# Kernel tuning notes

Hardware: AMD Instinct MI355X
Metric: run time of the kernel (lower is better)

Reference implementation:

```python
import jax, jax.numpy as jnp
import numpy as np

E = 800000
N = 50000
D = 128


def setup_inputs() -> dict:
    key = jax.random.key(0)
    k1, k2, k3, k4, k5 = jax.random.split(key, 5)
    messages = jax.random.normal(k1, (E, D), dtype=jnp.float32)
    dst_index = jax.random.randint(k2, (E,), 0, N, dtype=jnp.int32)
    h_prev = jax.random.normal(k3, (N, D), dtype=jnp.float32)
    # nn.Linear(5*D, D): weight [D, 5*D], bias [D]
    bound = 1.0 / np.sqrt(5 * D)
    W = jax.random.uniform(k4, (D, 5 * D), minval=-bound, maxval=bound, dtype=jnp.float32)
    b = jax.random.uniform(k5, (D,), minval=-bound, maxval=bound, dtype=jnp.float32)
    return {"messages": messages, "dst_index": dst_index, "h_prev": h_prev, "W": W, "b": b}


def reference(messages, dst_index, h_prev, W, b):
    n = h_prev.shape[0]
    ones = jnp.ones((messages.shape[0],), dtype=messages.dtype)
    count = jax.ops.segment_sum(ones, dst_index, num_segments=n)[:, None]       # [N,1]
    count_clamped = jnp.maximum(count, 1.0)
    sum_msg = jax.ops.segment_sum(messages, dst_index, num_segments=n)          # [N,D]
    mean_msg = sum_msg / count_clamped
    has_edge = count > 0
    # torch_scatter fills empty segments with 0 for max/min; segment_max/min give +/-inf
    max_msg = jnp.where(has_edge, jax.ops.segment_max(messages, dst_index, num_segments=n), 0.0)
    min_msg = jnp.where(has_edge, jax.ops.segment_min(messages, dst_index, num_segments=n), 0.0)
    sum_sq = jax.ops.segment_sum(messages * messages, dst_index, num_segments=n)
    mean_sq = sum_sq / count_clamped
    var = jnp.maximum(mean_sq - mean_msg * mean_msg, 1e-6)
    std_msg = jnp.sqrt(var)
    agg_feat = jnp.concatenate([mean_msg, max_msg, min_msg, std_msg, h_prev], axis=-1)  # [N,5D]
    return agg_feat @ W.T + b
```

## Files before the change

kernel.cpp:

```cpp
#include <hip/hip_runtime.h>
#include <hip/hip_bf16.h>
#include <cstdint>
#include <cstddef>

typedef unsigned short u16;
typedef __attribute__((ext_vector_type(8))) short short8;
typedef __attribute__((ext_vector_type(4))) float f32x4;

#define D_FEAT 128
#define CAP 64
#define NPB 32
#define ASTR 520

__global__ void zero_ints_kernel(int* __restrict__ a, int n) {
    int i = blockIdx.x * blockDim.x + threadIdx.x;
    int stride = gridDim.x * blockDim.x;
    for (; i < n; i += stride) a[i] = 0;
}

__global__ void wcvt_kernel(const float* __restrict__ W, u16* __restrict__ Wb, int n4) {
    int i = blockIdx.x * blockDim.x + threadIdx.x;
    if (i >= n4) return;
    float4 v = reinterpret_cast<const float4*>(W)[i];
    u16 o[4];
    float vv[4] = {v.x, v.y, v.z, v.w};
    #pragma unroll
    for (int t = 0; t < 4; ++t) {
        __hip_bfloat16 h = __float2bfloat16(vv[t]);
        o[t] = *reinterpret_cast<u16*>(&h);
    }
    reinterpret_cast<ushort2*>(Wb)[2 * i]     = make_ushort2(o[0], o[1]);
    reinterpret_cast<ushort2*>(Wb)[2 * i + 1] = make_ushort2(o[2], o[3]);
}

__global__ void scatter_kernel(const int* __restrict__ dst, int* __restrict__ cursor,
                               int* __restrict__ slots, int E) {
    int i = blockIdx.x * blockDim.x + threadIdx.x;
    int stride = gridDim.x * blockDim.x;
    for (; i < E; i += stride) {
        int d = dst[i];
        int p = atomicAdd(&cursor[d], 1);
        if (p < CAP) slots[(size_t)d * CAP + p] = i;
    }
}

__global__ __launch_bounds__(256) void fused_agg_gemm(
    const float* __restrict__ messages,
    const float* __restrict__ h_prev,
    const int* __restrict__ slots,
    const int* __restrict__ cursor,
    const u16* __restrict__ Wb,
    const float* __restrict__ bias,
    float* __restrict__ out,
    int N) {
    __shared__ __align__(16) u16 st[NPB * ASTR];

    const int wave = threadIdx.x >> 6;
    const int lane = threadIdx.x & 63;
    const int nb = blockIdx.x * NPB;

    for (int t = 0; t < NPB / 4; ++t) {
        const int nd = nb + wave * (NPB / 4) + t;
        if (nd >= N) break;
        const int cntT = cursor[nd];
        const int m = cntT < CAP ? cntT : CAP;
        const int* sl = slots + (size_t)nd * CAP;
        int eid = (lane < m) ? sl[lane] : 0;

        float s0 = 0.f, s1 = 0.f, q0 = 0.f, q1 = 0.f;
        float mx0 = -INFINITY, mx1 = -INFINITY, mn0 = INFINITY, mn1 = INFINITY;

        int i = 0;
        for (; i + 4 <= m; i += 4) {
            int e0 = __shfl(eid, i + 0, 64);
            int e1 = __shfl(eid, i + 1, 64);
            int e2 = __shfl(eid, i + 2, 64);
            int e3 = __shfl(eid, i + 3, 64);
            float2 v0 = *reinterpret_cast<const float2*>(messages + (size_t)e0 * D_FEAT + 2 * lane);
            float2 v1 = *reinterpret_cast<const float2*>(messages + (size_t)e1 * D_FEAT + 2 * lane);
            float2 v2 = *reinterpret_cast<const float2*>(messages + (size_t)e2 * D_FEAT + 2 * lane);
            float2 v3 = *reinterpret_cast<const float2*>(messages + (size_t)e3 * D_FEAT + 2 * lane);
            s0 += v0.x; q0 = fmaf(v0.x, v0.x, q0); mx0 = fmaxf(mx0, v0.x); mn0 = fminf(mn0, v0.x);
            s1 += v0.y; q1 = fmaf(v0.y, v0.y, q1); mx1 = fmaxf(mx1, v0.y); mn1 = fminf(mn1, v0.y);
            s0 += v1.x; q0 = fmaf(v1.x, v1.x, q0); mx0 = fmaxf(mx0, v1.x); mn0 = fminf(mn0, v1.x);
            s1 += v1.y; q1 = fmaf(v1.y, v1.y, q1); mx1 = fmaxf(mx1, v1.y); mn1 = fminf(mn1, v1.y);
            s0 += v2.x; q0 = fmaf(v2.x, v2.x, q0); mx0 = fmaxf(mx0, v2.x); mn0 = fminf(mn0, v2.x);
            s1 += v2.y; q1 = fmaf(v2.y, v2.y, q1); mx1 = fmaxf(mx1, v2.y); mn1 = fminf(mn1, v2.y);
            s0 += v3.x; q0 = fmaf(v3.x, v3.x, q0); mx0 = fmaxf(mx0, v3.x); mn0 = fminf(mn0, v3.x);
            s1 += v3.y; q1 = fmaf(v3.y, v3.y, q1); mx1 = fmaxf(mx1, v3.y); mn1 = fminf(mn1, v3.y);
        }
        for (; i < m; ++i) {
            int e = __shfl(eid, i, 64);
            float2 v = *reinterpret_cast<const float2*>(messages + (size_t)e * D_FEAT + 2 * lane);
            s0 += v.x; q0 = fmaf(v.x, v.x, q0); mx0 = fmaxf(mx0, v.x); mn0 = fminf(mn0, v.x);
            s1 += v.y; q1 = fmaf(v.y, v.y, q1); mx1 = fmaxf(mx1, v.y); mn1 = fminf(mn1, v.y);
        }

        float inv = 1.0f / fmaxf((float)cntT, 1.0f);
        float me0 = s0 * inv, me1 = s1 * inv;
        float var0 = fmaxf(q0 * inv - me0 * me0, 1e-6f);
        float var1 = fmaxf(q1 * inv - me1 * me1, 1e-6f);
        float sd0 = sqrtf(var0), sd1 = sqrtf(var1);
        if (cntT == 0) { mx0 = 0.f; mx1 = 0.f; mn0 = 0.f; mn1 = 0.f; }

        auto f2u = [](float x) -> unsigned {
            __hip_bfloat16 h = __float2bfloat16(x);
            return (unsigned)*reinterpret_cast<u16*>(&h);
        };
        unsigned* ag = reinterpret_cast<unsigned*>(st + (size_t)(nd - nb) * ASTR);
        ag[  0 + lane] = f2u(me0) | (f2u(me1) << 16);
        ag[ 64 + lane] = f2u(mx0) | (f2u(mx1) << 16);
        ag[128 + lane] = f2u(mn0) | (f2u(mn1) << 16);
        ag[192 + lane] = f2u(sd0) | (f2u(sd1) << 16);
    }
    __syncthreads();

    const int rt = (wave >> 1) * 16;
    const int c0 = (wave & 1) * 64;
    const int lr = lane & 15;
    const int kg = lane >> 4;

    const u16* aL = st + (size_t)(rt + lr) * ASTR + kg * 8;
    const int rowA = nb + rt + lr;
    const bool okA = rowA < N;
    const float* hp = h_prev + (size_t)rowA * D_FEAT + kg * 8;
    const u16* bp = Wb + (size_t)(c0 + lr) * 640 + kg * 8;

    f32x4 acc[4];
    #pragma unroll
    for (int ct = 0; ct < 4; ++ct) acc[ct] = (f32x4){0.f, 0.f, 0.f, 0.f};

    #pragma unroll 4
    for (int k0 = 0; k0 < 512; k0 += 32) {
        short8 a = *reinterpret_cast<const short8*>(aL + k0);
        #pragma unroll
        for (int ct = 0; ct < 4; ++ct) {
            short8 b = *reinterpret_cast<const short8*>(bp + (size_t)(ct * 16) * 640 + k0);
            acc[ct] = __builtin_amdgcn_mfma_f32_16x16x32_bf16(a, b, acc[ct], 0, 0, 0);
        }
    }

    auto cvt8 = [](const float* p) -> short8 {
        float4 x = *reinterpret_cast<const float4*>(p);
        float4 y = *reinterpret_cast<const float4*>(p + 4);
        float v[8] = {x.x, x.y, x.z, x.w, y.x, y.y, y.z, y.w};
        short8 r;
        #pragma unroll
        for (int t = 0; t < 8; ++t) {
            __hip_bfloat16 h = __float2bfloat16(v[t]);
            r[t] = *reinterpret_cast<short*>(&h);
        }
        return r;
    };
    #pragma unroll
    for (int kh = 0; kh < 128; kh += 32) {
        short8 a = {};
        if (okA) a = cvt8(hp + kh);
        #pragma unroll
        for (int ct = 0; ct < 4; ++ct) {
            short8 b = *reinterpret_cast<const short8*>(bp + (size_t)(ct * 16) * 640 + 512 + kh);
            acc[ct] = __builtin_amdgcn_mfma_f32_16x16x32_bf16(a, b, acc[ct], 0, 0, 0);
        }
    }

    #pragma unroll
    for (int ct = 0; ct < 4; ++ct) {
        int col = c0 + ct * 16 + lr;
        float bv = bias[col];
        #pragma unroll
        for (int j = 0; j < 4; ++j) {
            int row = nb + rt + kg * 4 + j;
            if (row < N) out[(size_t)row * D_FEAT + col] = acc[ct][j] + bv;
        }
    }
}

extern "C" void kernel_launch(void* const* d_in, const int* in_sizes, int n_in,
                              void* d_out, int out_size, void* d_ws, size_t ws_size,
                              hipStream_t stream) {
    const float* messages = (const float*)d_in[0];
    const int*   dst      = (const int*)d_in[1];
    const float* h_prev   = (const float*)d_in[2];
    const float* W        = (const float*)d_in[3];
    const float* bias     = (const float*)d_in[4];
    float* out = (float*)d_out;

    const int E = in_sizes[1];
    const int D = in_sizes[4];
    const int N = in_sizes[2] / D;
    const int WN = in_sizes[3];

    size_t off = 0;
    auto alloc = [&](size_t bytes) -> void* {
        void* p = (char*)d_ws + off;
        off += (bytes + 255) & ~(size_t)255;
        return p;
    };
    int* cursor = (int*)alloc((size_t)N * 4);
    int* slots  = (int*)alloc((size_t)N * CAP * 4);
    u16* Wb     = (u16*)alloc((size_t)WN * 2);
    (void)ws_size; (void)D;

    zero_ints_kernel<<<196, 256, 0, stream>>>(cursor, N);
    wcvt_kernel<<<(WN / 4 + 255) / 256, 256, 0, stream>>>(W, Wb, WN / 4);

    scatter_kernel<<<2048, 256, 0, stream>>>(dst, cursor, slots, E);

    fused_agg_gemm<<<(N + NPB - 1) / NPB, 256, 0, stream>>>(
        messages, h_prev, slots, cursor, Wb, bias, out, N);
}
```

Before: 245.1 us.

## Scatter bf16-packed messages into destination-sorted slots during the bucketing pass

The scatter pass no longer records edge indices. It streams the messages sequentially, converts them to bf16, and writes each row into a per-destination slot buffer. The aggregation kernel then reads contiguous, half-width rows per node instead of gathering fp32 rows by index. This aims to replace scattered fp32 gathers with sequential reads plus a compact contiguous re-read, at the cost of an extra scattered write pass, a very large workspace buffer, and bf16 rounding of messages before the sum, square, max and min statistics.

```diff
diff --git a/kernel.cpp b/kernel.cpp
--- a/kernel.cpp
+++ b/kernel.cpp
@@ -4,6 +4,7 @@
 #include <cstddef>
 
 typedef unsigned short u16;
+typedef unsigned int u32;
 typedef __attribute__((ext_vector_type(8))) short short8;
 typedef __attribute__((ext_vector_type(4))) float f32x4;
 
@@ -33,21 +34,55 @@
     reinterpret_cast<ushort2*>(Wb)[2 * i + 1] = make_ushort2(o[2], o[3]);
 }
 
-__global__ void scatter_kernel(const int* __restrict__ dst, int* __restrict__ cursor,
-                               int* __restrict__ slots, int E) {
-    int i = blockIdx.x * blockDim.x + threadIdx.x;
-    int stride = gridDim.x * blockDim.x;
-    for (; i < E; i += stride) {
-        int d = dst[i];
-        int p = atomicAdd(&cursor[d], 1);
-        if (p < CAP) slots[(size_t)d * CAP + p] = i;
+__device__ __forceinline__ u32 packbf16(float a, float b) {
+    __hip_bfloat16 ha = __float2bfloat16(a);
+    __hip_bfloat16 hb = __float2bfloat16(b);
+    return (u32)*reinterpret_cast<u16*>(&ha) | ((u32)*reinterpret_cast<u16*>(&hb) << 16);
+}
+
+__global__ __launch_bounds__(256) void scatter_convert(
+    const float* __restrict__ messages,
+    const int* __restrict__ dst,
+    int* __restrict__ cursor,
+    u32* __restrict__ msort,
+    int E) {
+    const int lane = threadIdx.x & 63;
+    const int gwave = (blockIdx.x * blockDim.x + threadIdx.x) >> 6;
+    const int nwaves = (gridDim.x * blockDim.x) >> 6;
+
+    for (int chunk = gwave * 64; chunk < E; chunk += nwaves * 64) {
+        int mE = E - chunk; if (mE > 64) mE = 64;
+        int d = 0, p = CAP;
+        if (lane < mE) {
+            d = dst[chunk + lane];
+            p = atomicAdd(&cursor[d], 1);
+        }
+        int i = 0;
+        for (; i + 4 <= mE; i += 4) {
+            int d0 = __shfl(d, i + 0, 64), p0 = __shfl(p, i + 0, 64);
+            int d1 = __shfl(d, i + 1, 64), p1 = __shfl(p, i + 1, 64);
+            int d2 = __shfl(d, i + 2, 64), p2 = __shfl(p, i + 2, 64);
+            int d3 = __shfl(d, i + 3, 64), p3 = __shfl(p, i + 3, 64);
+            float2 v0 = *reinterpret_cast<const float2*>(messages + (size_t)(chunk + i + 0) * D_FEAT + 2 * lane);
+            float2 v1 = *reinterpret_cast<const float2*>(messages + (size_t)(chunk + i + 1) * D_FEAT + 2 * lane);
+            float2 v2 = *reinterpret_cast<const float2*>(messages + (size_t)(chunk + i + 2) * D_FEAT + 2 * lane);
+            float2 v3 = *reinterpret_cast<const float2*>(messages + (size_t)(chunk + i + 3) * D_FEAT + 2 * lane);
+            if (p0 < CAP) msort[((size_t)d0 * CAP + p0) * 64 + lane] = packbf16(v0.x, v0.y);
+            if (p1 < CAP) msort[((size_t)d1 * CAP + p1) * 64 + lane] = packbf16(v1.x, v1.y);
+            if (p2 < CAP) msort[((size_t)d2 * CAP + p2) * 64 + lane] = packbf16(v2.x, v2.y);
+            if (p3 < CAP) msort[((size_t)d3 * CAP + p3) * 64 + lane] = packbf16(v3.x, v3.y);
+        }
+        for (; i < mE; ++i) {
+            int di = __shfl(d, i, 64), pi = __shfl(p, i, 64);
+            float2 v = *reinterpret_cast<const float2*>(messages + (size_t)(chunk + i) * D_FEAT + 2 * lane);
+            if (pi < CAP) msort[((size_t)di * CAP + pi) * 64 + lane] = packbf16(v.x, v.y);
+        }
     }
 }
 
 __global__ __launch_bounds__(256) void fused_agg_gemm(
-    const float* __restrict__ messages,
+    const u32* __restrict__ msort,
     const float* __restrict__ h_prev,
-    const int* __restrict__ slots,
     const int* __restrict__ cursor,
     const u16* __restrict__ Wb,
     const float* __restrict__ bias,
@@ -64,37 +99,32 @@
         if (nd >= N) break;
         const int cntT = cursor[nd];
         const int m = cntT < CAP ? cntT : CAP;
-        const int* sl = slots + (size_t)nd * CAP;
-        int eid = (lane < m) ? sl[lane] : 0;
+        const u32* base = msort + (size_t)nd * CAP * 64 + lane;
 
         float s0 = 0.f, s1 = 0.f, q0 = 0.f, q1 = 0.f;
         float mx0 = -INFINITY, mx1 = -INFINITY, mn0 = INFINITY, mn1 = INFINITY;
 
+        auto acc1 = [&](u32 u) {
+            float f0 = __uint_as_float(u << 16);
+            float f1 = __uint_as_float(u & 0xffff0000u);
+            s0 += f0; q0 = fmaf(f0, f0, q0); mx0 = fmaxf(mx0, f0); mn0 = fminf(mn0, f0);
+            s1 += f1; q1 = fmaf(f1, f1, q1); mx1 = fmaxf(mx1, f1); mn1 = fminf(mn1, f1);
+        };
+
         int i = 0;
-        for (; i + 4 <= m; i += 4) {
-            int e0 = __shfl(eid, i + 0, 64);
-            int e1 = __shfl(eid, i + 1, 64);
-            int e2 = __shfl(eid, i + 2, 64);
-            int e3 = __shfl(eid, i + 3, 64);
-            float2 v0 = *reinterpret_cast<const float2*>(messages + (size_t)e0 * D_FEAT + 2 * lane);
-            float2 v1 = *reinterpret_cast<const float2*>(messages + (size_t)e1 * D_FEAT + 2 * lane);
-            float2 v2 = *reinterpret_cast<const float2*>(messages + (size_t)e2 * D_FEAT + 2 * lane);
-            float2 v3 = *reinterpret_cast<const float2*>(messages + (size_t)e3 * D_FEAT + 2 * lane);
-            s0 += v0.x; q0 = fmaf(v0.x, v0.x, q0); mx0 = fmaxf(mx0, v0.x); mn0 = fminf(mn0, v0.x);
-            s1 += v0.y; q1 = fmaf(v0.y, v0.y, q1); mx1 = fmaxf(mx1, v0.y); mn1 = fminf(mn1, v0.y);
-            s0 += v1.x; q0 = fmaf(v1.x, v1.x, q0); mx0 = fmaxf(mx0, v1.x); mn0 = fminf(mn0, v1.x);
-            s1 += v1.y; q1 = fmaf(v1.y, v1.y, q1); mx1 = fmaxf(mx1, v1.y); mn1 = fminf(mn1, v1.y);
-            s0 += v2.x; q0 = fmaf(v2.x, v2.x, q0); mx0 = fmaxf(mx0, v2.x); mn0 = fminf(mn0, v2.x);
-            s1 += v2.y; q1 = fmaf(v2.y, v2.y, q1); mx1 = fmaxf(mx1, v2.y); mn1 = fminf(mn1, v2.y);
-            s0 += v3.x; q0 = fmaf(v3.x, v3.x, q0); mx0 = fmaxf(mx0, v3.x); mn0 = fminf(mn0, v3.x);
-            s1 += v3.y; q1 = fmaf(v3.y, v3.y, q1); mx1 = fmaxf(mx1, v3.y); mn1 = fminf(mn1, v3.y);
-        }
-        for (; i < m; ++i) {
-            int e = __shfl(eid, i, 64);
-            float2 v = *reinterpret_cast<const float2*>(messages + (size_t)e * D_FEAT + 2 * lane);
-            s0 += v.x; q0 = fmaf(v.x, v.x, q0); mx0 = fmaxf(mx0, v.x); mn0 = fminf(mn0, v.x);
-            s1 += v.y; q1 = fmaf(v.y, v.y, q1); mx1 = fmaxf(mx1, v.y); mn1 = fminf(mn1, v.y);
-        }
+        for (; i + 8 <= m; i += 8) {
+            u32 r0 = base[(size_t)(i + 0) * 64];
+            u32 r1 = base[(size_t)(i + 1) * 64];
+            u32 r2 = base[(size_t)(i + 2) * 64];
+            u32 r3 = base[(size_t)(i + 3) * 64];
+            u32 r4 = base[(size_t)(i + 4) * 64];
+            u32 r5 = base[(size_t)(i + 5) * 64];
+            u32 r6 = base[(size_t)(i + 6) * 64];
+            u32 r7 = base[(size_t)(i + 7) * 64];
+            acc1(r0); acc1(r1); acc1(r2); acc1(r3);
+            acc1(r4); acc1(r5); acc1(r6); acc1(r7);
+        }
+        for (; i < m; ++i) acc1(base[(size_t)i * 64]);
 
         float inv = 1.0f / fmaxf((float)cntT, 1.0f);
         float me0 = s0 * inv, me1 = s1 * inv;
@@ -103,15 +133,11 @@
         float sd0 = sqrtf(var0), sd1 = sqrtf(var1);
         if (cntT == 0) { mx0 = 0.f; mx1 = 0.f; mn0 = 0.f; mn1 = 0.f; }
 
-        auto f2u = [](float x) -> unsigned {
-            __hip_bfloat16 h = __float2bfloat16(x);
-            return (unsigned)*reinterpret_cast<u16*>(&h);
-        };
-        unsigned* ag = reinterpret_cast<unsigned*>(st + (size_t)(nd - nb) * ASTR);
-        ag[  0 + lane] = f2u(me0) | (f2u(me1) << 16);
-        ag[ 64 + lane] = f2u(mx0) | (f2u(mx1) << 16);
-        ag[128 + lane] = f2u(mn0) | (f2u(mn1) << 16);
-        ag[192 + lane] = f2u(sd0) | (f2u(sd1) << 16);
+        u32* ag = reinterpret_cast<u32*>(st + (size_t)(nd - nb) * ASTR);
+        ag[  0 + lane] = packbf16(me0, me1);
+        ag[ 64 + lane] = packbf16(mx0, mx1);
+        ag[128 + lane] = packbf16(mn0, mn1);
+        ag[192 + lane] = packbf16(sd0, sd1);
     }
     __syncthreads();
 
@@ -197,15 +223,15 @@
         return p;
     };
     int* cursor = (int*)alloc((size_t)N * 4);
-    int* slots  = (int*)alloc((size_t)N * CAP * 4);
+    u32* msort  = (u32*)alloc((size_t)N * CAP * 64 * 4);
     u16* Wb     = (u16*)alloc((size_t)WN * 2);
     (void)ws_size; (void)D;
 
     zero_ints_kernel<<<196, 256, 0, stream>>>(cursor, N);
     wcvt_kernel<<<(WN / 4 + 255) / 256, 256, 0, stream>>>(W, Wb, WN / 4);
 
-    scatter_kernel<<<2048, 256, 0, stream>>>(dst, cursor, slots, E);
+    scatter_convert<<<2048, 256, 0, stream>>>(messages, dst, cursor, msort, E);
 
     fused_agg_gemm<<<(N + NPB - 1) / NPB, 256, 0, stream>>>(
-        messages, h_prev, slots, cursor, Wb, bias, out, N);
-}
+        msort, h_prev, cursor, Wb, bias, out, N);
+}
```

After: 294.1 us. 20.0% more time.

## Process four nodes per wave in parallel with 16-lane groups and 32-byte loads

Applied to the files above, without the earlier changes.

The aggregation phase now splits each wave into four 16-lane quarters. Each quarter handles its own destination node, and each lane loads 8 floats per message row as two float4 loads instead of one float2. This puts more independent gather loads in flight per wave and raises load width, which suits a latency-bound irregular gather. The cost is divergence, because nodes in the same wave have different edge counts. There are also more accumulator registers, and the bf16 stores to shared memory are wider per lane.

```diff
diff --git a/kernel.cpp b/kernel.cpp
--- a/kernel.cpp
+++ b/kernel.cpp
@@ -4,6 +4,7 @@
 #include <cstddef>
 
 typedef unsigned short u16;
+typedef unsigned int u32;
 typedef __attribute__((ext_vector_type(8))) short short8;
 typedef __attribute__((ext_vector_type(4))) float f32x4;
 
@@ -31,6 +32,12 @@
     }
     reinterpret_cast<ushort2*>(Wb)[2 * i]     = make_ushort2(o[0], o[1]);
     reinterpret_cast<ushort2*>(Wb)[2 * i + 1] = make_ushort2(o[2], o[3]);
+}
+
+__device__ __forceinline__ u32 packbf16(float a, float b) {
+    __hip_bfloat16 ha = __float2bfloat16(a);
+    __hip_bfloat16 hb = __float2bfloat16(b);
+    return (u32)*reinterpret_cast<u16*>(&ha) | ((u32)*reinterpret_cast<u16*>(&hb) << 16);
 }
 
 __global__ void scatter_kernel(const int* __restrict__ dst, int* __restrict__ cursor,
@@ -41,6 +48,16 @@
         int d = dst[i];
         int p = atomicAdd(&cursor[d], 1);
         if (p < CAP) slots[(size_t)d * CAP + p] = i;
+    }
+}
+
+__device__ __forceinline__ void upd(f32x4& s, f32x4& q, f32x4& mx, f32x4& mn, f32x4 v) {
+    s += v;
+    q += v * v;
+    #pragma unroll
+    for (int j = 0; j < 4; ++j) {
+        mx[j] = fmaxf(mx[j], v[j]);
+        mn[j] = fminf(mn[j], v[j]);
     }
 }
 
@@ -57,61 +74,95 @@
 
     const int wave = threadIdx.x >> 6;
     const int lane = threadIdx.x & 63;
+    const int q = lane >> 4;
+    const int ql = lane & 15;
     const int nb = blockIdx.x * NPB;
 
-    for (int t = 0; t < NPB / 4; ++t) {
-        const int nd = nb + wave * (NPB / 4) + t;
-        if (nd >= N) break;
-        const int cntT = cursor[nd];
+    #pragma unroll
+    for (int t = 0; t < NPB / 16; ++t) {
+        const int nd = nb + wave * (NPB / 4) + t * 4 + q;
+        const bool ndok = nd < N;
+        const int cntT = ndok ? cursor[nd] : 0;
         const int m = cntT < CAP ? cntT : CAP;
         const int* sl = slots + (size_t)nd * CAP;
-        int eid = (lane < m) ? sl[lane] : 0;
-
-        float s0 = 0.f, s1 = 0.f, q0 = 0.f, q1 = 0.f;
-        float mx0 = -INFINITY, mx1 = -INFINITY, mn0 = INFINITY, mn1 = INFINITY;
-
-        int i = 0;
-        for (; i + 4 <= m; i += 4) {
-            int e0 = __shfl(eid, i + 0, 64);
-            int e1 = __shfl(eid, i + 1, 64);
-            int e2 = __shfl(eid, i + 2, 64);
-            int e3 = __shfl(eid, i + 3, 64);
-            float2 v0 = *reinterpret_cast<const float2*>(messages + (size_t)e0 * D_FEAT + 2 * lane);
-            float2 v1 = *reinterpret_cast<const float2*>(messages + (size_t)e1 * D_FEAT + 2 * lane);
-            float2 v2 = *reinterpret_cast<const float2*>(messages + (size_t)e2 * D_FEAT + 2 * lane);
-            float2 v3 = *reinterpret_cast<const float2*>(messages + (size_t)e3 * D_FEAT + 2 * lane);
-            s0 += v0.x; q0 = fmaf(v0.x, v0.x, q0); mx0 = fmaxf(mx0, v0.x); mn0 = fminf(mn0, v0.x);
-            s1 += v0.y; q1 = fmaf(v0.y, v0.y, q1); mx1 = fmaxf(mx1, v0.y); mn1 = fminf(mn1, v0.y);
-            s0 += v1.x; q0 = fmaf(v1.x, v1.x, q0); mx0 = fmaxf(mx0, v1.x); mn0 = fminf(mn0, v1.x);
-            s1 += v1.y; q1 = fmaf(v1.y, v1.y, q1); mx1 = fmaxf(mx1, v1.y); mn1 = fminf(mn1, v1.y);
-            s0 += v2.x; q0 = fmaf(v2.x, v2.x, q0); mx0 = fmaxf(mx0, v2.x); mn0 = fminf(mn0, v2.x);
-            s1 += v2.y; q1 = fmaf(v2.y, v2.y, q1); mx1 = fmaxf(mx1, v2.y); mn1 = fminf(mn1, v2.y);
-            s0 += v3.x; q0 = fmaf(v3.x, v3.x, q0); mx0 = fmaxf(mx0, v3.x); mn0 = fminf(mn0, v3.x);
-            s1 += v3.y; q1 = fmaf(v3.y, v3.y, q1); mx1 = fmaxf(mx1, v3.y); mn1 = fminf(mn1, v3.y);
-        }
-        for (; i < m; ++i) {
-            int e = __shfl(eid, i, 64);
-            float2 v = *reinterpret_cast<const float2*>(messages + (size_t)e * D_FEAT + 2 * lane);
-            s0 += v.x; q0 = fmaf(v.x, v.x, q0); mx0 = fmaxf(mx0, v.x); mn0 = fminf(mn0, v.x);
-            s1 += v.y; q1 = fmaf(v.y, v.y, q1); mx1 = fmaxf(mx1, v.y); mn1 = fminf(mn1, v.y);
+
+        f32x4 s0 = {0.f, 0.f, 0.f, 0.f}, s1 = {0.f, 0.f, 0.f, 0.f};
+        f32x4 q0 = {0.f, 0.f, 0.f, 0.f}, q1 = {0.f, 0.f, 0.f, 0.f};
+        f32x4 mx0 = {-INFINITY, -INFINITY, -INFINITY, -INFINITY};
+        f32x4 mx1 = mx0;
+        f32x4 mn0 = {INFINITY, INFINITY, INFINITY, INFINITY};
+        f32x4 mn1 = mn0;
+
+        for (int k0 = 0; k0 < m; k0 += 16) {
+            int mk = m - k0; if (mk > 16) mk = 16;
+            int eid = (k0 + ql < m) ? sl[k0 + ql] : 0;
+            int r = 0;
+            for (; r + 4 <= mk; r += 4) {
+                int e0 = __shfl(eid, 16 * q + r + 0, 64);
+                int e1 = __shfl(eid, 16 * q + r + 1, 64);
+                int e2 = __shfl(eid, 16 * q + r + 2, 64);
+                int e3 = __shfl(eid, 16 * q + r + 3, 64);
+                const float* p0 = messages + (size_t)e0 * D_FEAT + 8 * ql;
+                const float* p1 = messages + (size_t)e1 * D_FEAT + 8 * ql;
+                const float* p2 = messages + (size_t)e2 * D_FEAT + 8 * ql;
+                const float* p3 = messages + (size_t)e3 * D_FEAT + 8 * ql;
+                f32x4 a0 = *reinterpret_cast<const f32x4*>(p0);
+                f32x4 b0 = *reinterpret_cast<const f32x4*>(p0 + 4);
+                f32x4 a1 = *reinterpret_cast<const f32x4*>(p1);
+                f32x4 b1 = *reinterpret_cast<const f32x4*>(p1 + 4);
+                f32x4 a2 = *reinterpret_cast<const f32x4*>(p2);
+                f32x4 b2 = *reinterpret_cast<const f32x4*>(p2 + 4);
+                f32x4 a3 = *reinterpret_cast<const f32x4*>(p3);
+                f32x4 b3 = *reinterpret_cast<const f32x4*>(p3 + 4);
+                upd(s0, q0, mx0, mn0, a0); upd(s1, q1, mx1, mn1, b0);
+                upd(s0, q0, mx0, mn0, a1); upd(s1, q1, mx1, mn1, b1);
+                upd(s0, q0, mx0, mn0, a2); upd(s1, q1, mx1, mn1, b2);
+                upd(s0, q0, mx0, mn0, a3); upd(s1, q1, mx1, mn1, b3);
+            }
+            for (; r < mk; ++r) {
+                int e = __shfl(eid, 16 * q + r, 64);
+                const float* p = messages + (size_t)e * D_FEAT + 8 * ql;
+                f32x4 a = *reinterpret_cast<const f32x4*>(p);
+                f32x4 b = *reinterpret_cast<const f32x4*>(p + 4);
+                upd(s0, q0, mx0, mn0, a); upd(s1, q1, mx1, mn1, b);
+            }
         }
 
         float inv = 1.0f / fmaxf((float)cntT, 1.0f);
-        float me0 = s0 * inv, me1 = s1 * inv;
-        float var0 = fmaxf(q0 * inv - me0 * me0, 1e-6f);
-        float var1 = fmaxf(q1 * inv - me1 * me1, 1e-6f);
-        float sd0 = sqrtf(var0), sd1 = sqrtf(var1);
-        if (cntT == 0) { mx0 = 0.f; mx1 = 0.f; mn0 = 0.f; mn1 = 0.f; }
-
-        auto f2u = [](float x) -> unsigned {
-            __hip_bfloat16 h = __float2bfloat16(x);
-            return (unsigned)*reinterpret_cast<u16*>(&h);
-        };
-        unsigned* ag = reinterpret_cast<unsigned*>(st + (size_t)(nd - nb) * ASTR);
-        ag[  0 + lane] = f2u(me0) | (f2u(me1) << 16);
-        ag[ 64 + lane] = f2u(mx0) | (f2u(mx1) << 16);
-        ag[128 + lane] = f2u(mn0) | (f2u(mn1) << 16);
-        ag[192 + lane] = f2u(sd0) | (f2u(sd1) << 16);
+        f32x4 meA = s0 * inv, meB = s1 * inv;
+        f32x4 vA = q0 * inv - meA * meA;
+        f32x4 vB = q1 * inv - meB * meB;
+        f32x4 sdA, sdB;
+        #pragma unroll
+        for (int j = 0; j < 4; ++j) {
+            sdA[j] = sqrtf(fmaxf(vA[j], 1e-6f));
+            sdB[j] = sqrtf(fmaxf(vB[j], 1e-6f));
+        }
+        if (cntT == 0) {
+            mx0 = (f32x4){0.f, 0.f, 0.f, 0.f}; mx1 = mx0;
+            mn0 = mx0; mn1 = mx0;
+        }
+
+        if (ndok) {
+            u32* ag = reinterpret_cast<u32*>(st + (size_t)(nd - nb) * ASTR);
+            const int wi = 4 * ql;
+            ag[  0 + wi + 0] = packbf16(meA[0], meA[1]);
+            ag[  0 + wi + 1] = packbf16(meA[2], meA[3]);
+            ag[  0 + wi + 2] = packbf16(meB[0], meB[1]);
+            ag[  0 + wi + 3] = packbf16(meB[2], meB[3]);
+            ag[ 64 + wi + 0] = packbf16(mx0[0], mx0[1]);
+            ag[ 64 + wi + 1] = packbf16(mx0[2], mx0[3]);
+            ag[ 64 + wi + 2] = packbf16(mx1[0], mx1[1]);
+            ag[ 64 + wi + 3] = packbf16(mx1[2], mx1[3]);
+            ag[128 + wi + 0] = packbf16(mn0[0], mn0[1]);
+            ag[128 + wi + 1] = packbf16(mn0[2], mn0[3]);
+            ag[128 + wi + 2] = packbf16(mn1[0], mn1[1]);
+            ag[128 + wi + 3] = packbf16(mn1[2], mn1[3]);
+            ag[192 + wi + 0] = packbf16(sdA[0], sdA[1]);
+            ag[192 + wi + 1] = packbf16(sdA[2], sdA[3]);
+            ag[192 + wi + 2] = packbf16(sdB[0], sdB[1]);
+            ag[192 + wi + 3] = packbf16(sdB[2], sdB[3]);
+        }
     }
     __syncthreads();
 
```

New measurement: 221.6 us. -9.6%, faster.
